# Performance work log

Measured on AMD Instinct MI355X. Metric: run time of the kernel, lower is better.

The kernel has to match this reference:

```python
import jax, jax.numpy as jnp
import numpy as np

EPS = 1e-05
FACT = 2.0
REJECT_RATIO = 1.0


def setup_inputs() -> dict:
    key = jax.random.key(0)
    k1, k2 = jax.random.split(key)
    B, N = 8, 4096
    pc1 = jax.random.normal(k1, (B, 4, N), dtype=jnp.float32)
    pc2 = jax.random.normal(k2, (B, 4, N), dtype=jnp.float32)
    # homogeneous coordinates: last row = 1
    pc1 = pc1.at[:, 3, :].set(1.0)
    pc2 = pc2.at[:, 3, :].set(1.0)
    return {"pc1": pc1, "pc2": pc2}


def _rot_to_quat(R):
    # standard rotation-matrix -> quaternion (w, x, y, z)
    r00, r11, r22 = R[0, 0], R[1, 1], R[2, 2]
    qw = 0.5 * jnp.sqrt(jnp.maximum(1e-12, 1.0 + r00 + r11 + r22))
    qx = 0.5 * jnp.sqrt(jnp.maximum(0.0, 1.0 + r00 - r11 - r22))
    qy = 0.5 * jnp.sqrt(jnp.maximum(0.0, 1.0 - r00 + r11 - r22))
    qz = 0.5 * jnp.sqrt(jnp.maximum(0.0, 1.0 - r00 - r11 + r22))
    qx = jnp.where(R[2, 1] - R[1, 2] < 0, -qx, qx)
    qy = jnp.where(R[0, 2] - R[2, 0] < 0, -qy, qy)
    qz = jnp.where(R[1, 0] - R[0, 1] < 0, -qz, qz)
    return jnp.stack([qw, qx, qy, qz])


def _normalize_rotmat(R):
    # operates on COLUMNS, like the torch code (R[:, 2] etc.)
    z = R[:, 2] / jnp.linalg.norm(R[:, 2])
    y = R[:, 1]
    x = jnp.cross(y, z)
    x = x / jnp.linalg.norm(x)
    y = jnp.cross(z, x)
    return jnp.stack([x, y, z], axis=1)


def _norm_tf(pc):
    # T = diag(1/std) @ [I | -mean]  (std is unbiased, as torch.std)
    std = jnp.std(pc[:3, :], axis=1, ddof=1)
    mean = jnp.mean(pc[:3, :], axis=1)
    T = jnp.zeros((4, 4), dtype=pc.dtype)
    T = T.at[jnp.arange(3), jnp.arange(3)].set(1.0 / std)
    T = T.at[:3, 3].set(-mean / std)
    T = T.at[3, 3].set(1.0)
    return T


def _per_sample(pc1, pc2):
    # ---- soft_knn: pairwise squared distance over xyz ----
    p1, p2 = pc1[:3], pc2[:3]  # (3, N)
    d = ((p1 ** 2).sum(0)[:, None]
         - 2.0 * jnp.einsum('dn,dm->nm', p1, p2)
         + (p2 ** 2).sum(0)[None, :])            # (N1, N2)
    W = jax.nn.softmax(FACT / jnp.clip(d, EPS, None), axis=1)
    pc_nearest = pc2 @ W.T                        # (4, N1) soft-gathered points

    # ---- soft_outlier_rejection ----
    dist = jnp.linalg.norm(pc1 - pc_nearest, axis=0)
    filt = jax.nn.sigmoid((dist - dist.mean() * REJECT_RATIO - EPS) * -1e10)

    # ---- dlt(pc1, pc_nearest, filt) ----
    T2 = _norm_tf(pc_nearest)
    pc2n = T2 @ pc_nearest
    T1 = _norm_tf(pc1)
    pc1n = T1 @ pc1

    mask = (filt > 0.5).astype(pc1.dtype)         # hard inlier mask (sigmoid slope 1e10)
    N = pc1.shape[1]
    a = pc1n.T                                    # (N, 4)
    z4 = jnp.zeros((N, 4), dtype=pc1.dtype)
    row0 = jnp.concatenate([z4, -pc2n[2][:, None] * a, pc2n[1][:, None] * a], axis=1)
    row1 = jnp.concatenate([pc2n[2][:, None] * a, z4, -pc2n[0][:, None] * a], axis=1)
    M = (jnp.stack([row0, row1], axis=1) * mask[:, None, None]).reshape(2 * N, 12)

    _, _, Vh = jnp.linalg.svd(M, full_matrices=False)
    p = Vh[-1]                                    # null-space vector (12,)
    p = jnp.where(p[10] < 0, -p, p)
    p = p / jnp.sqrt(p[8] ** 2 + p[9] ** 2 + p[10] ** 2)

    T = jnp.zeros((4, 4), dtype=pc1.dtype)
    T = T.at[:3, :].set(p.reshape(3, 4)).at[3, 3].set(1.0)
    T = jnp.linalg.inv(T2) @ T @ T1
    R = _normalize_rotmat(T[:3, :3])
    T = T.at[:3, :3].set(R)
    return T, _rot_to_quat(R), T[:3, 3]


def reference(pc1, pc2):
    T, q, t = jax.vmap(_per_sample)(pc1, pc2)
    return T, q, t
```

## Files before the change

kernel.cpp:

```cpp
#include <hip/hip_runtime.h>
#include <math.h>

#define NPTS 4096
#define EPSC 1e-5f
#define F2C (2.0f*1.44269504088896340736f)

#if __has_builtin(__builtin_amdgcn_exp2f)
#define FEXP2 __builtin_amdgcn_exp2f
#else
#define FEXP2(x) __expf((x)*0.6931471805599453f)
#endif

#define IDX(i,j) ((i)*((i)+1)/2 + (j))

typedef float f2 __attribute__((ext_vector_type(2)));
__device__ __forceinline__ f2 splat2(float v){ f2 r; r.x=v; r.y=v; return r; }

__global__ void __launch_bounds__(256) k_soft(const float* __restrict__ pc1,
                                              const float* __restrict__ pc2,
                                              float* __restrict__ part){
  constexpr int CHN = 256, NC = 16;
  int bid = blockIdx.x;
  int chunk = bid & (NC-1), rb = (bid/NC) & 15, b = bid/(NC*16);

  __shared__ float xs[CHN], ys[CHN], zs[CHN], ws[CHN];
  {
    const float* p2 = pc2 + (size_t)b*4*NPTS + chunk*CHN;
    for (int m = threadIdx.x; m < CHN; m += 256){
      float x = p2[m], y = p2[m+NPTS], z = p2[m+2*NPTS];
      xs[m]=x; ys[m]=y; zs[m]=z; ws[m]=x*x+y*y+z*z;
    }
  }
  __syncthreads();

  int n = rb*256 + threadIdx.x;
  const float* p1 = pc1 + (size_t)b*4*NPTS + n;
  float x1 = p1[0], y1 = p1[NPTS], z1 = p1[2*NPTS];
  float q1 = x1*x1 + y1*y1 + z1*z1;
  f2 mx = splat2(-2.f*x1), my = splat2(-2.f*y1), mz = splat2(-2.f*z1);
  f2 q12 = splat2(q1), eps2 = splat2(EPSC);

  f2 cx = *(const f2*)&xs[0], cy = *(const f2*)&ys[0];
  f2 cz = *(const f2*)&zs[0], cw = *(const f2*)&ws[0];
  f2 d = cw + q12;
  d = __builtin_elementwise_fma(mz, cz, d);
  d = __builtin_elementwise_fma(my, cy, d);
  d = __builtin_elementwise_fma(mx, cx, d);
  d = __builtin_elementwise_max(d, eps2);
  f2 r; r.x = __builtin_amdgcn_rcpf(d.x); r.y = __builtin_amdgcn_rcpf(d.y);
  f2 s = splat2(F2C) * r;
  float m_ = fmaxf(s.x, s.y);
  f2 t = s - splat2(m_);
  f2 pe; pe.x = FEXP2(t.x); pe.y = FEXP2(t.y);
  f2 L2 = pe;
  f2 Ax2 = pe*cx, Ay2 = pe*cy, Az2 = pe*cz;

  #pragma unroll 8
  for (int p=1; p<CHN/2; ++p){
    cx = *(const f2*)&xs[2*p]; cy = *(const f2*)&ys[2*p];
    cz = *(const f2*)&zs[2*p]; cw = *(const f2*)&ws[2*p];
    d = cw + q12;
    d = __builtin_elementwise_fma(mz, cz, d);
    d = __builtin_elementwise_fma(my, cy, d);
    d = __builtin_elementwise_fma(mx, cx, d);
    d = __builtin_elementwise_max(d, eps2);
    r.x = __builtin_amdgcn_rcpf(d.x); r.y = __builtin_amdgcn_rcpf(d.y);
    t = __builtin_elementwise_fma(splat2(F2C), r, splat2(-m_));
    float tmax = fmaxf(t.x, t.y);
    if (__any(tmax > 0.f)){
      float tp = fmaxf(tmax, 0.f);
      float sc = FEXP2(-tp);
      L2 *= sc; Ax2 *= sc; Ay2 *= sc; Az2 *= sc;
      m_ += tp;
      t = t - splat2(tp);
    }
    pe.x = FEXP2(t.x); pe.y = FEXP2(t.y);
    L2 += pe;
    Ax2 = __builtin_elementwise_fma(pe, cx, Ax2);
    Ay2 = __builtin_elementwise_fma(pe, cy, Ay2);
    Az2 = __builtin_elementwise_fma(pe, cz, Az2);
  }
  float L  = L2.x + L2.y;
  float Ax = Ax2.x + Ax2.y;
  float Ay = Ay2.x + Ay2.y;
  float Az = Az2.x + Az2.y;

  float* pp = part + ((size_t)(b*NC + chunk)*5)*NPTS + n;
  pp[0]=m_; pp[NPTS]=L; pp[2*NPTS]=Ax; pp[3*NPTS]=Ay; pp[4*NPTS]=Az;
}

template<int NC>
__global__ void __launch_bounds__(512) k_merge(const float* __restrict__ pc1,
                                               const float* __restrict__ part,
                                               float* __restrict__ pcn,
                                               float* __restrict__ dist,
                                               float* __restrict__ psum13){
  int b = blockIdx.x >> 4, rb = blockIdx.x & 15;
  int t = threadIdx.x & 255, half = threadIdx.x >> 8;
  int n = rb*256 + t;
  constexpr int H = NC/2;
  float sc[H], Lc[H], Axc[H], Ayc[H], Azc[H];
  float S = -3.4e38f;
  #pragma unroll
  for (int c=0;c<H;c++){
    const float* pp = part + ((size_t)(b*NC + half*H + c)*5)*NPTS + n;
    sc[c]=pp[0]; Lc[c]=pp[NPTS]; Axc[c]=pp[2*NPTS]; Ayc[c]=pp[3*NPTS]; Azc[c]=pp[4*NPTS];
    S = fmaxf(S, sc[c]);
  }
  float L=0.f, Ax=0.f, Ay=0.f, Az=0.f;
  #pragma unroll
  for (int c=0;c<H;c++){
    float w = FEXP2(sc[c]-S);
    L=fmaf(w,Lc[c],L); Ax=fmaf(w,Axc[c],Ax); Ay=fmaf(w,Ayc[c],Ay); Az=fmaf(w,Azc[c],Az);
  }
  __shared__ float ex[256][5];
  if (half==1){ ex[t][0]=S; ex[t][1]=L; ex[t][2]=Ax; ex[t][3]=Ay; ex[t][4]=Az; }
  __syncthreads();
  __shared__ float red[4][13];
  if (half==0){
    float S1=ex[t][0];
    float M = fmaxf(S,S1);
    float w0=FEXP2(S-M), w1=FEXP2(S1-M);
    L = w0*L + w1*ex[t][1];
    Ax = w0*Ax + w1*ex[t][2];
    Ay = w0*Ay + w1*ex[t][3];
    Az = w0*Az + w1*ex[t][4];
    float inv = 1.f/L;
    float px=Ax*inv, py=Ay*inv, pz=Az*inv;
    const float* p1 = pc1 + (size_t)b*4*NPTS + n;
    float x1=p1[0], y1=p1[NPTS], z1=p1[2*NPTS];
    float dx=x1-px, dy=y1-py, dz=z1-pz;
    float dd=sqrtf(dx*dx+dy*dy+dz*dz);
    pcn[(size_t)(b*3+0)*NPTS+n]=px;
    pcn[(size_t)(b*3+1)*NPTS+n]=py;
    pcn[(size_t)(b*3+2)*NPTS+n]=pz;
    dist[(size_t)b*NPTS+n]=dd;
    float acc[13]={x1,y1,z1,x1*x1,y1*y1,z1*z1,px,py,pz,px*px,py*py,pz*pz,dd};
    int lane = t & 63, wv = t >> 6;
    #pragma unroll
    for (int k=0;k<13;k++){
      float v = acc[k];
      v += __shfl_xor(v,32); v += __shfl_xor(v,16); v += __shfl_xor(v,8);
      v += __shfl_xor(v,4);  v += __shfl_xor(v,2);  v += __shfl_xor(v,1);
      if (lane==0) red[wv][k]=v;
    }
  }
  __syncthreads();
  if (threadIdx.x<13)
    psum13[(size_t)blockIdx.x*13 + threadIdx.x] =
      red[0][threadIdx.x]+red[1][threadIdx.x]+red[2][threadIdx.x]+red[3][threadIdx.x];
}

__device__ __forceinline__ float elemA(const float* S, int i, int k){
  int bi=i>>2, bj=k>>2;
  int ii=i&3, jj=k&3;
  int lo = ii<jj?ii:jj, hi = ii<jj?jj:ii;
  int pe = 4*lo - ((lo*(lo-1))>>1) + (hi-lo);
  int w;
  if (bi==bj) w = (bi==2)?30:0;
  else {
    int blo = bi<bj?bi:bj, bhi = bi<bj?bj:bi;
    if (blo==0 && bhi==1) return 0.f;
    w = (blo==0)?10:20;
  }
  return S[w+pe];
}

__global__ void __launch_bounds__(256) k_solve(const float* __restrict__ pc1,
                                               const float* __restrict__ pcn,
                                               const float* __restrict__ dist,
                                               const float* __restrict__ psum13,
                                               float* __restrict__ out){
  int b=blockIdx.x, t=threadIdx.x;
  __shared__ float stot[13];
  __shared__ float sst[13];
  if (t<13){
    float s=0.f;
    #pragma unroll
    for (int i=0;i<16;i++) s += psum13[(size_t)(b*16+i)*13 + t];
    stot[t]=s;
  }
  __syncthreads();
  if (t==0){
    const float Nf = 4096.f, Nm1 = 4095.f;
    #pragma unroll
    for (int j=0;j<3;j++){
      float m  = stot[j]/Nf;
      float v  = (stot[3+j]-Nf*m*m)/Nm1;
      sst[j]=m; sst[3+j]=sqrtf(fmaxf(v,0.f));
      float m2 = stot[6+j]/Nf;
      float v2 = (stot[9+j]-Nf*m2*m2)/Nm1;
      sst[6+j]=m2; sst[9+j]=sqrtf(fmaxf(v2,0.f));
    }
    sst[12]=stot[12]/Nf;
  }
  __syncthreads();
  float i1x=1.f/sst[3], i1y=1.f/sst[4], i1z=1.f/sst[5];
  float t1x=-sst[0]/sst[3], t1y=-sst[1]/sst[4], t1z=-sst[2]/sst[5];
  float i2x=1.f/sst[9], i2y=1.f/sst[10], i2z=1.f/sst[11];
  float t2x=-sst[6]/sst[9], t2y=-sst[7]/sst[10], t2z=-sst[8]/sst[11];
  float meanD=sst[12];

  float acc[40];
  #pragma unroll
  for (int k=0;k<40;k++) acc[k]=0.f;
  #pragma unroll 4
  for (int i=0;i<16;i++){
    int n=i*256+t;
    const float* p1 = pc1 + (size_t)b*4*NPTS + n;
    float X1=fmaf(p1[0],i1x,t1x), Y1=fmaf(p1[NPTS],i1y,t1y), Z1=fmaf(p1[2*NPTS],i1z,t1z);
    float X2=fmaf(pcn[(size_t)(b*3+0)*NPTS+n],i2x,t2x);
    float Y2=fmaf(pcn[(size_t)(b*3+1)*NPTS+n],i2y,t2y);
    float Z2=fmaf(pcn[(size_t)(b*3+2)*NPTS+n],i2z,t2z);
    float zthr = (dist[(size_t)b*NPTS+n] - meanD) - EPSC;
    float msk = (zthr < 0.f) ? 1.f : 0.f;
    float tz = msk*Z2;
    float wA = tz*Z2, wB = -tz*X2, wC = -tz*Y2;
    float wD = msk*fmaf(X2,X2,Y2*Y2);
    float ee[10]={X1*X1, X1*Y1, X1*Z1, X1, Y1*Y1, Y1*Z1, Y1, Z1*Z1, Z1, 1.f};
    #pragma unroll
    for (int j=0;j<10;j++){
      acc[j]    = fmaf(wA,ee[j],acc[j]);
      acc[10+j] = fmaf(wB,ee[j],acc[10+j]);
      acc[20+j] = fmaf(wC,ee[j],acc[20+j]);
      acc[30+j] = fmaf(wD,ee[j],acc[30+j]);
    }
  }
  __shared__ float red[4][40];
  __shared__ float SS[40];
  {
    int lane=t&63, wv=t>>6;
    #pragma unroll
    for (int k=0;k<40;k++){
      float v=acc[k];
      v+=__shfl_xor(v,32); v+=__shfl_xor(v,16); v+=__shfl_xor(v,8);
      v+=__shfl_xor(v,4);  v+=__shfl_xor(v,2);  v+=__shfl_xor(v,1);
      if(lane==0) red[wv][k]=v;
    }
  }
  __syncthreads();
  if (t<40) SS[t]=red[0][t]+red[1][t]+red[2][t]+red[3][t];
  __syncthreads();

  if (t<64){
    float a[78];
    #pragma unroll
    for (int i=0;i<12;i++)
      #pragma unroll
      for (int j=0;j<=i;j++)
        a[IDX(i,j)] = elemA(SS,i,j);
    {
      float tr=0.f;
      #pragma unroll
      for (int i=0;i<12;i++) tr += a[IDX(i,i)];
      float eps = 1e-5f * tr * (1.f/12.f);
      #pragma unroll
      for (int i=0;i<12;i++) a[IDX(i,i)] += eps;
    }
    #pragma unroll
    for (int j=0;j<12;j++){
      float s = a[IDX(j,j)];
      #pragma unroll
      for (int k=0;k<j;k++) s = fmaf(-a[IDX(j,k)], a[IDX(j,k)], s);
      float d = sqrtf(fmaxf(s, 1e-30f));
      a[IDX(j,j)] = d;
      float dinv = __builtin_amdgcn_rcpf(d);
      #pragma unroll
      for (int i=j+1;i<12;i++){
        float s2 = a[IDX(i,j)];
        #pragma unroll
        for (int k=0;k<j;k++) s2 = fmaf(-a[IDX(i,k)], a[IDX(j,k)], s2);
        a[IDX(i,j)] = s2 * dinv;
      }
    }
    float y[12], Brow[12];
    #pragma unroll
    for (int i=0;i<12;i++){
      float s = (i==t) ? 1.f : 0.f;
      #pragma unroll
      for (int k=0;k<i;k++) s = fmaf(-a[IDX(i,k)], y[k], s);
      y[i] = s * __builtin_amdgcn_rcpf(a[IDX(i,i)]);
    }
    #pragma unroll
    for (int i=11;i>=0;i--){
      float s = y[i];
      #pragma unroll
      for (int k=11;k>i;k--) s = fmaf(-a[IDX(k,i)], Brow[k], s);
      Brow[i] = s * __builtin_amdgcn_rcpf(a[IDX(i,i)]);
    }
    {
      float mxv = 0.f;
      #pragma unroll
      for (int i=0;i<12;i++) mxv = fmaxf(mxv, fabsf(Brow[i]));
      mxv = fmaxf(mxv, __shfl_xor(mxv,1)); mxv = fmaxf(mxv, __shfl_xor(mxv,2));
      mxv = fmaxf(mxv, __shfl_xor(mxv,4)); mxv = fmaxf(mxv, __shfl_xor(mxv,8));
      float sc = __builtin_amdgcn_rcpf(mxv);
      #pragma unroll
      for (int i=0;i<12;i++) Brow[i] *= sc;
    }
    #pragma unroll
    for (int rep=0; rep<2; ++rep){
      float nr[12];
      #pragma unroll
      for (int i=0;i<12;i++) nr[i]=0.f;
      #pragma unroll
      for (int k=0;k<12;k++){
        float bjk = Brow[k];
        #pragma unroll
        for (int m2=0;m2<12;m2++){
          float bkm = __shfl(Brow[m2], k);
          nr[m2] = fmaf(bjk, bkm, nr[m2]);
        }
      }
      float mxv = 0.f;
      #pragma unroll
      for (int i=0;i<12;i++) mxv = fmaxf(mxv, fabsf(nr[i]));
      mxv = fmaxf(mxv, __shfl_xor(mxv,1)); mxv = fmaxf(mxv, __shfl_xor(mxv,2));
      mxv = fmaxf(mxv, __shfl_xor(mxv,4)); mxv = fmaxf(mxv, __shfl_xor(mxv,8));
      float sc = __builtin_amdgcn_rcpf(mxv);
      #pragma unroll
      for (int i=0;i<12;i++) Brow[i] = nr[i]*sc;
    }
    float v = 0.f;
    #pragma unroll
    for (int i=0;i<12;i++) v += Brow[i];
    #pragma unroll
    for (int it=0; it<14; ++it){
      float w = 0.f;
      #pragma unroll
      for (int k=0;k<12;k++) w = fmaf(Brow[k], __shfl(v,k), w);
      float nn = w*w;
      nn += __shfl_xor(nn,1); nn += __shfl_xor(nn,2);
      nn += __shfl_xor(nn,4); nn += __shfl_xor(nn,8);
      v = w * rsqrtf(nn);
    }
    float pvf[12];
    #pragma unroll
    for (int i=0;i<12;i++) pvf[i] = __shfl(v, i);

    if (t==0){
      double pv[12];
      #pragma unroll
      for (int i=0;i<12;i++) pv[i]=(double)pvf[i];
      if (pv[10]<0.0){
        #pragma unroll
        for (int i=0;i<12;i++) pv[i]=-pv[i];
      }
      double nrm = sqrt(pv[8]*pv[8]+pv[9]*pv[9]+pv[10]*pv[10]);
      #pragma unroll
      for (int i=0;i<12;i++) pv[i]/=nrm;
      double m1[3]={sst[0],sst[1],sst[2]}, sd1[3]={sst[3],sst[4],sst[5]};
      double m2[3]={sst[6],sst[7],sst[8]}, sd2[3]={sst[9],sst[10],sst[11]};
      double Td[3][4]={{pv[0],pv[1],pv[2],pv[3]},
                       {pv[4],pv[5],pv[6],pv[7]},
                       {pv[8],pv[9],pv[10],pv[11]}};
      double F[3][4];
      for (int i=0;i<3;i++){
        double b3 = Td[i][3];
        for (int j=0;j<3;j++){
          F[i][j] = sd2[i]*(Td[i][j]/sd1[j]);
          b3 += Td[i][j]*(-m1[j]/sd1[j]);
        }
        F[i][3] = sd2[i]*b3 + m2[i];
      }
      double zx=F[0][2],zy=F[1][2],zz2=F[2][2];
      double zn=sqrt(zx*zx+zy*zy+zz2*zz2);
      zx/=zn; zy/=zn; zz2/=zn;
      double yx=F[0][1],yy=F[1][1],yz=F[2][1];
      double xx=yy*zz2-yz*zy, xy=yz*zx-yx*zz2, xz=yx*zy-yy*zx;
      double xn=sqrt(xx*xx+xy*xy+xz*xz);
      xx/=xn; xy/=xn; xz/=xn;
      double y2x=zy*xz-zz2*xy, y2y=zz2*xx-zx*xz, y2z=zx*xy-zy*xx;
      double R00=xx,R01=y2x,R02=zx;
      double R10=xy,R11=y2y,R12=zy;
      double R20=xz,R21=y2z,R22=zz2;
      float* oT = out + b*16;
      oT[0]=(float)R00; oT[1]=(float)R01; oT[2]=(float)R02; oT[3]=(float)F[0][3];
      oT[4]=(float)R10; oT[5]=(float)R11; oT[6]=(float)R12; oT[7]=(float)F[1][3];
      oT[8]=(float)R20; oT[9]=(float)R21; oT[10]=(float)R22; oT[11]=(float)F[2][3];
      oT[12]=0.f; oT[13]=0.f; oT[14]=0.f; oT[15]=1.f;
      double qw=0.5*sqrt(fmax(1e-12, 1.0+R00+R11+R22));
      double qx=0.5*sqrt(fmax(0.0, 1.0+R00-R11-R22));
      double qy=0.5*sqrt(fmax(0.0, 1.0-R00+R11-R22));
      double qz=0.5*sqrt(fmax(0.0, 1.0-R00-R11+R22));
      if (R21-R12<0.0) qx=-qx;
      if (R02-R20<0.0) qy=-qy;
      if (R10-R01<0.0) qz=-qz;
      float* oQ = out + 128 + b*4;
      oQ[0]=(float)qw; oQ[1]=(float)qx; oQ[2]=(float)qy; oQ[3]=(float)qz;
      float* ot3 = out + 160 + b*3;
      ot3[0]=(float)F[0][3]; ot3[1]=(float)F[1][3]; ot3[2]=(float)F[2][3];
    }
  }
}

extern "C" void kernel_launch(void* const* d_in, const int* in_sizes, int n_in,
                              void* d_out, int out_size, void* d_ws, size_t ws_size,
                              hipStream_t stream) {
  const float* pc1 = (const float*)d_in[0];
  const float* pc2 = (const float*)d_in[1];
  float* out  = (float*)d_out;
  float* ws   = (float*)d_ws;

  float* part  = ws;
  float* pcn   = part + 2621440;
  float* dist  = pcn + 98304;
  float* psum13= dist + 32768;

  hipLaunchKernelGGL(k_soft,      dim3(2048), dim3(256), 0, stream, pc1, pc2, part);
  hipLaunchKernelGGL(k_merge<16>, dim3(128),  dim3(512), 0, stream, pc1, part, pcn, dist, psum13);
  hipLaunchKernelGGL(k_solve,     dim3(8),    dim3(256), 0, stream, pc1, pcn, dist, psum13, out);
}
```

Baseline: 146.4 us.

## Skip negligible softmax groups in soft-kNN via distance threshold

The soft-kNN inner loop now processes four candidates per iteration and computes a distance threshold from the running max logit minus a margin. When every lane's candidates in a group lie beyond that threshold, their exp contributions would be below 2^-40 relative to the max, so the reciprocal, exp and accumulation work is skipped for the whole wavefront. This saves transcendental and FMA work when the max logit is large. The cost is an extra min reduction and a wavefront vote per group, and skipped terms introduce a tiny approximation error.

After: 160.4 us. +9.5%, slower.

```diff
diff --git a/kernel.cpp b/kernel.cpp
--- a/kernel.cpp
+++ b/kernel.cpp
@@ -4,6 +4,7 @@
 #define NPTS 4096
 #define EPSC 1e-5f
 #define F2C (2.0f*1.44269504088896340736f)
+#define MARGIN 40.0f
 
 #if __has_builtin(__builtin_amdgcn_exp2f)
 #define FEXP2 __builtin_amdgcn_exp2f
@@ -39,46 +40,90 @@
   float q1 = x1*x1 + y1*y1 + z1*z1;
   f2 mx = splat2(-2.f*x1), my = splat2(-2.f*y1), mz = splat2(-2.f*z1);
   f2 q12 = splat2(q1), eps2 = splat2(EPSC);
-
-  f2 cx = *(const f2*)&xs[0], cy = *(const f2*)&ys[0];
-  f2 cz = *(const f2*)&zs[0], cw = *(const f2*)&ws[0];
-  f2 d = cw + q12;
-  d = __builtin_elementwise_fma(mz, cz, d);
-  d = __builtin_elementwise_fma(my, cy, d);
-  d = __builtin_elementwise_fma(mx, cx, d);
-  d = __builtin_elementwise_max(d, eps2);
-  f2 r; r.x = __builtin_amdgcn_rcpf(d.x); r.y = __builtin_amdgcn_rcpf(d.y);
-  f2 s = splat2(F2C) * r;
-  float m_ = fmaxf(s.x, s.y);
-  f2 t = s - splat2(m_);
-  f2 pe; pe.x = FEXP2(t.x); pe.y = FEXP2(t.y);
-  f2 L2 = pe;
-  f2 Ax2 = pe*cx, Ay2 = pe*cy, Az2 = pe*cz;
-
-  #pragma unroll 8
-  for (int p=1; p<CHN/2; ++p){
-    cx = *(const f2*)&xs[2*p]; cy = *(const f2*)&ys[2*p];
-    cz = *(const f2*)&zs[2*p]; cw = *(const f2*)&ws[2*p];
-    d = cw + q12;
-    d = __builtin_elementwise_fma(mz, cz, d);
-    d = __builtin_elementwise_fma(my, cy, d);
-    d = __builtin_elementwise_fma(mx, cx, d);
-    d = __builtin_elementwise_max(d, eps2);
-    r.x = __builtin_amdgcn_rcpf(d.x); r.y = __builtin_amdgcn_rcpf(d.y);
-    t = __builtin_elementwise_fma(splat2(F2C), r, splat2(-m_));
-    float tmax = fmaxf(t.x, t.y);
+  const f2 F22 = splat2(F2C);
+
+  f2 ax = *(const f2*)&xs[0], bx = *(const f2*)&xs[2];
+  f2 ay = *(const f2*)&ys[0], by = *(const f2*)&ys[2];
+  f2 az = *(const f2*)&zs[0], bz = *(const f2*)&zs[2];
+  f2 aw = *(const f2*)&ws[0], bw = *(const f2*)&ws[2];
+  f2 da = aw + q12;
+  da = __builtin_elementwise_fma(mz, az, da);
+  da = __builtin_elementwise_fma(my, ay, da);
+  da = __builtin_elementwise_fma(mx, ax, da);
+  f2 db = bw + q12;
+  db = __builtin_elementwise_fma(mz, bz, db);
+  db = __builtin_elementwise_fma(my, by, db);
+  db = __builtin_elementwise_fma(mx, bx, db);
+  da = __builtin_elementwise_max(da, eps2);
+  db = __builtin_elementwise_max(db, eps2);
+  f2 ra, rbv;
+  ra.x  = __builtin_amdgcn_rcpf(da.x); ra.y  = __builtin_amdgcn_rcpf(da.y);
+  rbv.x = __builtin_amdgcn_rcpf(db.x); rbv.y = __builtin_amdgcn_rcpf(db.y);
+  f2 sa = F22*ra, sb = F22*rbv;
+  f2 sm = __builtin_elementwise_max(sa, sb);
+  float m_ = fmaxf(sm.x, sm.y);
+  f2 nm2 = splat2(-m_);
+  f2 ta = sa + nm2, tb = sb + nm2;
+  f2 pea, peb;
+  pea.x = FEXP2(ta.x); pea.y = FEXP2(ta.y);
+  peb.x = FEXP2(tb.x); peb.y = FEXP2(tb.y);
+  f2 L2 = pea + peb;
+  f2 Ax2 = pea*ax + peb*bx;
+  f2 Ay2 = pea*ay + peb*by;
+  f2 Az2 = pea*az + peb*bz;
+
+  float r40 = m_ - MARGIN;
+  float d_thr = (r40 > 0.f) ? F2C*__builtin_amdgcn_rcpf(r40) : 3.4e38f;
+
+  #pragma unroll 2
+  for (int g=1; g<CHN/4; ++g){
+    int c0 = g*4;
+    ax = *(const f2*)&xs[c0];   bx = *(const f2*)&xs[c0+2];
+    ay = *(const f2*)&ys[c0];   by = *(const f2*)&ys[c0+2];
+    az = *(const f2*)&zs[c0];   bz = *(const f2*)&zs[c0+2];
+    aw = *(const f2*)&ws[c0];   bw = *(const f2*)&ws[c0+2];
+    da = aw + q12;
+    da = __builtin_elementwise_fma(mz, az, da);
+    da = __builtin_elementwise_fma(my, ay, da);
+    da = __builtin_elementwise_fma(mx, ax, da);
+    db = bw + q12;
+    db = __builtin_elementwise_fma(mz, bz, db);
+    db = __builtin_elementwise_fma(my, by, db);
+    db = __builtin_elementwise_fma(mx, bx, db);
+    f2 mm = __builtin_elementwise_min(da, db);
+    float gmin = fminf(mm.x, mm.y);
+    if (__all(gmin > d_thr)) continue;
+
+    da = __builtin_elementwise_max(da, eps2);
+    db = __builtin_elementwise_max(db, eps2);
+    ra.x  = __builtin_amdgcn_rcpf(da.x); ra.y  = __builtin_amdgcn_rcpf(da.y);
+    rbv.x = __builtin_amdgcn_rcpf(db.x); rbv.y = __builtin_amdgcn_rcpf(db.y);
+    ta = __builtin_elementwise_fma(F22, ra,  nm2);
+    tb = __builtin_elementwise_fma(F22, rbv, nm2);
+    f2 tm2 = __builtin_elementwise_max(ta, tb);
+    float tmax = fmaxf(tm2.x, tm2.y);
     if (__any(tmax > 0.f)){
       float tp = fmaxf(tmax, 0.f);
       float sc = FEXP2(-tp);
       L2 *= sc; Ax2 *= sc; Ay2 *= sc; Az2 *= sc;
       m_ += tp;
-      t = t - splat2(tp);
-    }
-    pe.x = FEXP2(t.x); pe.y = FEXP2(t.y);
-    L2 += pe;
-    Ax2 = __builtin_elementwise_fma(pe, cx, Ax2);
-    Ay2 = __builtin_elementwise_fma(pe, cy, Ay2);
-    Az2 = __builtin_elementwise_fma(pe, cz, Az2);
+      nm2 = splat2(-m_);
+      ta = ta - splat2(tp);
+      tb = tb - splat2(tp);
+      float r40n = m_ - MARGIN;
+      d_thr = (r40n > 0.f) ? F2C*__builtin_amdgcn_rcpf(r40n) : 3.4e38f;
+    }
+    ta = __builtin_elementwise_min(ta, splat2(0.f));
+    tb = __builtin_elementwise_min(tb, splat2(0.f));
+    pea.x = FEXP2(ta.x); pea.y = FEXP2(ta.y);
+    peb.x = FEXP2(tb.x); peb.y = FEXP2(tb.y);
+    L2 += pea + peb;
+    Ax2 = __builtin_elementwise_fma(pea, ax, Ax2);
+    Ax2 = __builtin_elementwise_fma(peb, bx, Ax2);
+    Ay2 = __builtin_elementwise_fma(pea, ay, Ay2);
+    Ay2 = __builtin_elementwise_fma(peb, by, Ay2);
+    Az2 = __builtin_elementwise_fma(pea, az, Az2);
+    Az2 = __builtin_elementwise_fma(peb, bz, Az2);
   }
   float L  = L2.x + L2.y;
   float Ax = Ax2.x + Ax2.y;
```
